# Kernel tuning notes

Measured on AMD Instinct MI355X. Metric: run time of the kernel, lower is better.

The kernel has to match this reference:

```python
import jax, jax.numpy as jnp
import numpy as np

DIST_THRESHOLD = 0.1  # distance_threshold from __init__
NO_CODE_ID = -1


def setup_inputs() -> dict:
    key = jax.random.key(0)
    k1, k2 = jax.random.split(key)
    x = jax.random.normal(k1, (16, 4096, 64), dtype=jnp.float32)
    codes = jax.random.normal(k2, (4096, 64), dtype=jnp.float32)  # active codebook rows
    return {"x": x, "codes": codes}


def reference(x, codes):
    # Squared Euclidean distance (cdist ** 2) via the expansion
    x2 = jnp.sum(x * x, axis=-1, keepdims=True)            # [B, N, 1]
    c2 = jnp.sum(codes * codes, axis=-1)                    # [M]
    d2 = x2 + c2 - 2.0 * jnp.einsum("bnd,md->bnm", x, codes)  # [B, N, M]
    within = jnp.any(d2 <= DIST_THRESHOLD, axis=-1)         # [B, N]
    nn_ids = jnp.argmin(d2, axis=-1)                        # [B, N]
    return jnp.where(within, nn_ids, NO_CODE_ID)
```

## Files before the change

kernel.cpp:

```cpp
#include <hip/hip_runtime.h>
#include <stdint.h>

typedef float f32x4 __attribute__((ext_vector_type(4)));
typedef __bf16 bf16x8 __attribute__((ext_vector_type(8)));
typedef __bf16 bf16x4 __attribute__((ext_vector_type(4)));

#define NROWS 65536
#define NCODES 4096
#define NDIM 64
#define STEPS 128
#define SSTEP 2
#define PHASES (STEPS / SSTEP)
#define BIAS 2048.0f
#define CBMASK 0x7FFFF


__device__ __forceinline__ void gld_lds16(const void* g, void* l) {
  __builtin_amdgcn_global_load_lds(
      (const __attribute__((address_space(1))) unsigned int*)g,
      (__attribute__((address_space(3))) unsigned int*)l, 16, 0, 0);
}

__device__ __forceinline__ uint32_t umin2(uint32_t a, uint32_t b) {
  return a < b ? a : b;
}

__global__ __launch_bounds__(256) void prep_codes_k(const float* __restrict__ codes,
                                                    float* __restrict__ nc2p,
                                                    __bf16* __restrict__ cb) {
  const int t = blockIdx.x * 256 + threadIdx.x;
  f32x4 v = *(const f32x4*)(codes + t * 4);
  bf16x4 o;
  float s = 0.f;
#pragma unroll
  for (int j = 0; j < 4; j++) {
    o[j] = (__bf16)v[j];
    s += v[j] * v[j];
  }
  *(bf16x4*)(cb + t * 4) = o;
  s += __shfl_xor(s, 1);
  s += __shfl_xor(s, 2);
  s += __shfl_xor(s, 4);
  s += __shfl_xor(s, 8);
  if ((threadIdx.x & 15) == 0) {
    const int c = t >> 4;
    const int pidx = (c >> 5) * 16 + (c & 15);
    const int half = (c >> 4) & 1;
    nc2p[pidx * 2 + half] = -0.5f * s - BIAS;
  }
}

__global__ __launch_bounds__(256, 6) void nn_main(const float* __restrict__ x,
                                                  const __bf16* __restrict__ cbv,
                                                  const float2* __restrict__ nc2p,
                                                  int* __restrict__ out) {
  const int tid  = threadIdx.x;
  const int lane = tid & 63;
  const int w    = tid >> 6;
  const int col  = lane & 15;
  const int quad = lane >> 4;
  const int bid  = blockIdx.x;
  const int rowbase = bid * 128 + w * 32;
  const int s0 = bid & 127;
  const char* cbb = (const char*)cbv;

  __shared__ __align__(16) char stage[2][SSTEP * 4096];
  __shared__ __align__(8) float2 ncl[2048];

  const uint32_t schunk = ((uint32_t)(tid * 16)) ^ ((((uint32_t)tid >> 3) & 7u) << 4);
  const char* srcbase = cbb + schunk;
  const uint32_t rot = (uint32_t)s0 * 4096u;
#pragma unroll
  for (int i = 0; i < 4; i++)
    gld_lds16((const char*)nc2p + i * 4096 + tid * 16,
              (char*)ncl + i * 4096 + w * 1024);
#pragma unroll
  for (int i = 0; i < SSTEP; i++)
    gld_lds16(srcbase + ((rot + i * 4096u) & CBMASK),
              &stage[0][i * 4096 + w * 1024]);

  bf16x8 a[2][2];
  float x2part[2];
#pragma unroll
  for (int rt = 0; rt < 2; rt++) {
    const float* xr = x + (rowbase + rt * 16 + col) * NDIM + quad * 8;
    float p = 0.f;
#pragma unroll
    for (int kc = 0; kc < 2; kc++) {
      f32x4 v0 = *(const f32x4*)(xr + kc * 32);
      f32x4 v1 = *(const f32x4*)(xr + kc * 32 + 4);
      bf16x8 af;
#pragma unroll
      for (int j = 0; j < 4; j++) {
        af[j]     = (__bf16)v0[j];
        af[j + 4] = (__bf16)v1[j];
        p += v0[j] * v0[j] + v1[j] * v1[j];
      }
      a[rt][kc] = af;
    }
    x2part[rt] = p;
  }
#pragma unroll
  for (int rt = 0; rt < 2; rt++) {
    float p = x2part[rt];
    p += __shfl_xor(p, 16);
    p += __shfl_xor(p, 32);
    x2part[rt] = p;
  }

  uint32_t bestK[2][4];
#pragma unroll
  for (int rt = 0; rt < 2; rt++)
#pragma unroll
    for (int j = 0; j < 4; j++) bestK[rt][j] = 0xFFFFFFFFu;

  const uint32_t swz = ((uint32_t)(col & 7)) << 4;
  const uint32_t o00 = ((uint32_t)(col * 128 + quad * 16)) ^ swz;
  const uint32_t o01 = ((uint32_t)(col * 128 + 64 + quad * 16)) ^ swz;
  const uint32_t o10 = ((uint32_t)(2048 + col * 128 + quad * 16)) ^ swz;
  const uint32_t o11 = ((uint32_t)(2048 + col * 128 + 64 + quad * 16)) ^ swz;

  __syncthreads();

#pragma unroll 1
  for (int p = 0; p < PHASES; ++p) {
    if (p < PHASES - 1) {
      const uint32_t pb = rot + (uint32_t)(p + 1) * (SSTEP * 4096u);
      char* dst = &stage[(p + 1) & 1][w * 1024];
#pragma unroll
      for (int i = 0; i < SSTEP; i++)
        gld_lds16(srcbase + ((pb + i * 4096u) & CBMASK), dst + i * 4096);
    }
    const char* sb = stage[p & 1];
#pragma unroll
    for (int ss = 0; ss < SSTEP; ss++) {
      const int s_eff = (s0 + p * SSTEP + ss) & 127;
      const float2 nv = ncl[s_eff * 16 + col];
      bf16x8 b00 = *(const bf16x8*)(sb + ss * 4096 + o00);
      bf16x8 b01 = *(const bf16x8*)(sb + ss * 4096 + o01);
      bf16x8 b10 = *(const bf16x8*)(sb + ss * 4096 + o10);
      bf16x8 b11 = *(const bf16x8*)(sb + ss * 4096 + o11);
      f32x4 ci0 = {nv.x, nv.x, nv.x, nv.x};
      f32x4 ci1 = {nv.y, nv.y, nv.y, nv.y};
      const uint32_t vk0 = (uint32_t)(col | (s_eff << 5));
      const uint32_t vk1 = vk0 | 16u;
#pragma unroll
      for (int rt = 0; rt < 2; rt++) {
        f32x4 acc0 = __builtin_amdgcn_mfma_f32_16x16x32_bf16(a[rt][0], b00, ci0, 0, 0, 0);
        acc0 = __builtin_amdgcn_mfma_f32_16x16x32_bf16(a[rt][1], b01, acc0, 0, 0, 0);
        f32x4 acc1 = __builtin_amdgcn_mfma_f32_16x16x32_bf16(a[rt][0], b10, ci1, 0, 0, 0);
        acc1 = __builtin_amdgcn_mfma_f32_16x16x32_bf16(a[rt][1], b11, acc1, 0, 0, 0);
#pragma unroll
        for (int j = 0; j < 4; j++) {
          const uint32_t k0 = (__builtin_bit_cast(uint32_t, acc0[j]) & 0xFFFFF000u) | vk0;
          const uint32_t k1 = (__builtin_bit_cast(uint32_t, acc1[j]) & 0xFFFFF000u) | vk1;
          bestK[rt][j] = umin2(bestK[rt][j], umin2(k0, k1));
        }
      }
    }
    __syncthreads();
  }

#pragma unroll
  for (int rt = 0; rt < 2; rt++) {
#pragma unroll
    for (int j = 0; j < 4; j++) {
      uint32_t bk = bestK[rt][j];
#pragma unroll
      for (int off = 1; off < 16; off <<= 1) {
        const uint32_t ok = (uint32_t)__shfl_xor((int)bk, off);
        bk = umin2(bk, ok);
      }
      const float x2v = __shfl(x2part[rt], (lane & 48) + quad * 4 + j);
      if (col == 0) {
        const float Tp = __builtin_bit_cast(float, bk & 0xFFFFF000u);
        const float d2 = fmaf(-2.0f, Tp, x2v) - 2.0f * BIAS;
        out[rowbase + rt * 16 + quad * 4 + j] =
            (d2 <= 0.1f) ? (int)(bk & 4095u) : -1;
      }
    }
  }
}

extern "C" void kernel_launch(void* const* d_in, const int* in_sizes, int n_in,
                              void* d_out, int out_size, void* d_ws, size_t ws_size,
                              hipStream_t stream) {
  const float* x = (const float*)d_in[0];
  const float* codes = (const float*)d_in[1];
  int* out = (int*)d_out;

  char* ws = (char*)d_ws;
  __bf16* cb = (__bf16*)ws;
  float* nc2p = (float*)(ws + 0x080000);

  prep_codes_k<<<256, 256, 0, stream>>>(codes, nc2p, cb);
  nn_main<<<512, 256, 0, stream>>>(x, cb, (const float2*)nc2p, out);
}
```

Measured before the change: 99.28 us.

## Use 512-thread blocks with one 16-row tile per wave

Doubles the block to 8 waves and gives each wave one 16-row tile instead of two, so every staged codebook chunk in LDS is shared by more waves and each thread issues one async load per phase. Per-thread register use (A fragments, bestK) halves, which may allow more resident waves. The cost is half as much MFMA work per B-fragment LDS read, a higher LDS-read-to-compute ratio, and barriers that now synchronise more waves. The starting rotation s0 now only takes even values.

Result: slower. 101.9 us (+2.6%).

```diff
diff --git a/kernel.cpp b/kernel.cpp
--- a/kernel.cpp
+++ b/kernel.cpp
@@ -50,7 +50,7 @@
   }
 }
 
-__global__ __launch_bounds__(256, 6) void nn_main(const float* __restrict__ x,
+__global__ __launch_bounds__(512, 4) void nn_main(const float* __restrict__ x,
                                                   const __bf16* __restrict__ cbv,
                                                   const float2* __restrict__ nc2p,
                                                   int* __restrict__ out) {
@@ -60,8 +60,8 @@
   const int col  = lane & 15;
   const int quad = lane >> 4;
   const int bid  = blockIdx.x;
-  const int rowbase = bid * 128 + w * 32;
-  const int s0 = bid & 127;
+  const int rowbase = bid * 128 + w * 16;
+  const int s0 = (bid & 63) * 2;
   const char* cbb = (const char*)cbv;
 
   __shared__ __align__(16) char stage[2][SSTEP * 4096];
@@ -71,19 +71,15 @@
   const char* srcbase = cbb + schunk;
   const uint32_t rot = (uint32_t)s0 * 4096u;
 #pragma unroll
-  for (int i = 0; i < 4; i++)
-    gld_lds16((const char*)nc2p + i * 4096 + tid * 16,
-              (char*)ncl + i * 4096 + w * 1024);
-#pragma unroll
-  for (int i = 0; i < SSTEP; i++)
-    gld_lds16(srcbase + ((rot + i * 4096u) & CBMASK),
-              &stage[0][i * 4096 + w * 1024]);
+  for (int i = 0; i < 2; i++)
+    gld_lds16((const char*)nc2p + i * 8192 + w * 1024 + lane * 16,
+              (char*)ncl + i * 8192 + w * 1024);
+  gld_lds16(srcbase + rot, &stage[0][w * 1024]);
 
-  bf16x8 a[2][2];
-  float x2part[2];
-#pragma unroll
-  for (int rt = 0; rt < 2; rt++) {
-    const float* xr = x + (rowbase + rt * 16 + col) * NDIM + quad * 8;
+  bf16x8 a[2];
+  float x2part;
+  {
+    const float* xr = x + (rowbase + col) * NDIM + quad * 8;
     float p = 0.f;
 #pragma unroll
     for (int kc = 0; kc < 2; kc++) {
@@ -96,23 +92,16 @@
         af[j + 4] = (__bf16)v1[j];
         p += v0[j] * v0[j] + v1[j] * v1[j];
       }
-      a[rt][kc] = af;
+      a[kc] = af;
     }
-    x2part[rt] = p;
-  }
-#pragma unroll
-  for (int rt = 0; rt < 2; rt++) {
-    float p = x2part[rt];
     p += __shfl_xor(p, 16);
     p += __shfl_xor(p, 32);
-    x2part[rt] = p;
+    x2part = p;
   }
 
-  uint32_t bestK[2][4];
+  uint32_t bestK[4];
 #pragma unroll
-  for (int rt = 0; rt < 2; rt++)
-#pragma unroll
-    for (int j = 0; j < 4; j++) bestK[rt][j] = 0xFFFFFFFFu;
+  for (int j = 0; j < 4; j++) bestK[j] = 0xFFFFFFFFu;
 
   const uint32_t swz = ((uint32_t)(col & 7)) << 4;
   const uint32_t o00 = ((uint32_t)(col * 128 + quad * 16)) ^ swz;
@@ -125,11 +114,8 @@
 #pragma unroll 1
   for (int p = 0; p < PHASES; ++p) {
     if (p < PHASES - 1) {
-      const uint32_t pb = rot + (uint32_t)(p + 1) * (SSTEP * 4096u);
-      char* dst = &stage[(p + 1) & 1][w * 1024];
-#pragma unroll
-      for (int i = 0; i < SSTEP; i++)
-        gld_lds16(srcbase + ((pb + i * 4096u) & CBMASK), dst + i * 4096);
+      const uint32_t pb = (rot + (uint32_t)(p + 1) * 8192u) & CBMASK;
+      gld_lds16(srcbase + pb, &stage[(p + 1) & 1][w * 1024]);
     }
     const char* sb = stage[p & 1];
 #pragma unroll
@@ -144,40 +130,33 @@
       f32x4 ci1 = {nv.y, nv.y, nv.y, nv.y};
       const uint32_t vk0 = (uint32_t)(col | (s_eff << 5));
       const uint32_t vk1 = vk0 | 16u;
+      f32x4 acc0 = __builtin_amdgcn_mfma_f32_16x16x32_bf16(a[0], b00, ci0, 0, 0, 0);
+      acc0 = __builtin_amdgcn_mfma_f32_16x16x32_bf16(a[1], b01, acc0, 0, 0, 0);
+      f32x4 acc1 = __builtin_amdgcn_mfma_f32_16x16x32_bf16(a[0], b10, ci1, 0, 0, 0);
+      acc1 = __builtin_amdgcn_mfma_f32_16x16x32_bf16(a[1], b11, acc1, 0, 0, 0);
 #pragma unroll
-      for (int rt = 0; rt < 2; rt++) {
-        f32x4 acc0 = __builtin_amdgcn_mfma_f32_16x16x32_bf16(a[rt][0], b00, ci0, 0, 0, 0);
-        acc0 = __builtin_amdgcn_mfma_f32_16x16x32_bf16(a[rt][1], b01, acc0, 0, 0, 0);
-        f32x4 acc1 = __builtin_amdgcn_mfma_f32_16x16x32_bf16(a[rt][0], b10, ci1, 0, 0, 0);
-        acc1 = __builtin_amdgcn_mfma_f32_16x16x32_bf16(a[rt][1], b11, acc1, 0, 0, 0);
-#pragma unroll
-        for (int j = 0; j < 4; j++) {
-          const uint32_t k0 = (__builtin_bit_cast(uint32_t, acc0[j]) & 0xFFFFF000u) | vk0;
-          const uint32_t k1 = (__builtin_bit_cast(uint32_t, acc1[j]) & 0xFFFFF000u) | vk1;
-          bestK[rt][j] = umin2(bestK[rt][j], umin2(k0, k1));
-        }
+      for (int j = 0; j < 4; j++) {
+        const uint32_t k0 = (__builtin_bit_cast(uint32_t, acc0[j]) & 0xFFFFF000u) | vk0;
+        const uint32_t k1 = (__builtin_bit_cast(uint32_t, acc1[j]) & 0xFFFFF000u) | vk1;
+        bestK[j] = umin2(bestK[j], umin2(k0, k1));
       }
     }
     __syncthreads();
   }
 
 #pragma unroll
-  for (int rt = 0; rt < 2; rt++) {
+  for (int j = 0; j < 4; j++) {
+    uint32_t bk = bestK[j];
 #pragma unroll
-    for (int j = 0; j < 4; j++) {
-      uint32_t bk = bestK[rt][j];
-#pragma unroll
-      for (int off = 1; off < 16; off <<= 1) {
-        const uint32_t ok = (uint32_t)__shfl_xor((int)bk, off);
-        bk = umin2(bk, ok);
-      }
-      const float x2v = __shfl(x2part[rt], (lane & 48) + quad * 4 + j);
-      if (col == 0) {
-        const float Tp = __builtin_bit_cast(float, bk & 0xFFFFF000u);
-        const float d2 = fmaf(-2.0f, Tp, x2v) - 2.0f * BIAS;
-        out[rowbase + rt * 16 + quad * 4 + j] =
-            (d2 <= 0.1f) ? (int)(bk & 4095u) : -1;
-      }
+    for (int off = 1; off < 16; off <<= 1) {
+      const uint32_t ok = (uint32_t)__shfl_xor((int)bk, off);
+      bk = umin2(bk, ok);
+    }
+    const float x2v = __shfl(x2part, (lane & 48) + quad * 4 + j);
+    if (col == 0) {
+      const float Tp = __builtin_bit_cast(float, bk & 0xFFFFF000u);
+      const float d2 = fmaf(-2.0f, Tp, x2v) - 2.0f * BIAS;
+      out[rowbase + quad * 4 + j] = (d2 <= 0.1f) ? (int)(bk & 4095u) : -1;
     }
   }
 }
@@ -194,5 +173,5 @@
   float* nc2p = (float*)(ws + 0x080000);
 
   prep_codes_k<<<256, 256, 0, stream>>>(codes, nc2p, cb);
-  nn_main<<<512, 256, 0, stream>>>(x, cb, (const float2*)nc2p, out);
+  nn_main<<<512, 512, 0, stream>>>(x, cb, (const float2*)nc2p, out);
 }
```
